# Kernel tuning notes

Measured on AMD Instinct MI355X. Metric: run time of the kernel, lower is better.

Reference implementation:

```python
import jax, jax.numpy as jnp
import numpy as np

H = 1024   # lstm_size
Z = 512    # z_size
E = 32     # subseq_embedding_dim
B = 256    # batch
T = 64     # length


def setup_inputs() -> dict:
    key = jax.random.key(0)
    ks = jax.random.split(key, 16)
    k = 1.0 / np.sqrt(H)  # PyTorch default uniform init bound
    u = lambda kk, shape: jax.random.uniform(kk, shape, jnp.float32, -k, k)
    return {
        "z": jax.random.normal(ks[0], (1, B, Z), jnp.float32),
        "targets": jax.random.normal(ks[1], (T, B, E), jnp.float32),
        "length": T,
        # LSTM layer 0 (input E -> H), gate order i,f,g,o as in PyTorch
        "W_ih0": u(ks[2], (4 * H, E)), "W_hh0": u(ks[3], (4 * H, H)),
        "b_ih0": u(ks[4], (4 * H,)),   "b_hh0": u(ks[5], (4 * H,)),
        # LSTM layer 1 (input H -> H)
        "W_ih1": u(ks[6], (4 * H, H)), "W_hh1": u(ks[7], (4 * H, H)),
        "b_ih1": u(ks[8], (4 * H,)),   "b_hh1": u(ks[9], (4 * H,)),
        # per-layer z -> initial hidden projections
        "Wz0": u(ks[10], (H, Z)), "bz0": u(ks[11], (H,)),
        "Wz1": u(ks[12], (H, Z)), "bz1": u(ks[13], (H,)),
        # output projection H -> E
        "Wp": u(ks[14], (E, H)), "bp": u(ks[15], (E,)),
    }


def _lstm_cell(x, h, c, W_ih, W_hh, b_ih, b_hh):
    # gates: [i, f, g, o] stacked along last dim (PyTorch layout)
    g = x @ W_ih.T + h @ W_hh.T + (b_ih + b_hh)
    i, f, gg, o = jnp.split(g, 4, axis=-1)
    c2 = jax.nn.sigmoid(f) * c + jax.nn.sigmoid(i) * jnp.tanh(gg)
    h2 = jax.nn.sigmoid(o) * jnp.tanh(c2)
    return h2, c2


def reference(z, targets, length, W_ih0, W_hh0, b_ih0, b_hh0,
              W_ih1, W_hh1, b_ih1, b_hh1, Wz0, bz0, Wz1, bz1, Wp, bp):
    batch = z.shape[1]
    emb = targets.shape[-1]
    z0 = z[0]  # (B, Z)
    # initial hidden = tanh(Linear(z)) per layer, initial cell = zeros
    h0 = jnp.tanh(z0 @ Wz0.T + bz0)
    h1 = jnp.tanh(z0 @ Wz1.T + bz1)
    c0 = jnp.zeros_like(h0)
    c1 = jnp.zeros_like(h1)

    # teacher-forced inputs: step 0 is zeros, step t uses targets[t-1] (detached)
    inputs = jnp.concatenate(
        [jnp.zeros((1, batch, emb), targets.dtype),
         jax.lax.stop_gradient(targets[: length - 1])], axis=0)

    def step(carry, x):
        h0, c0, h1, c1 = carry
        h0, c0 = _lstm_cell(x, h0, c0, W_ih0, W_hh0, b_ih0, b_hh0)
        h1, c1 = _lstm_cell(h0, h1, c1, W_ih1, W_hh1, b_ih1, b_hh1)
        out = h1 @ Wp.T + bp  # (B, E)
        return (h0, c0, h1, c1), out

    _, outs = jax.lax.scan(step, (h0, c0, h1, c1), inputs)
    return outs  # (length, B, E) == embedding_outputs
```

## Files before the change

### kernel.cpp

```cpp
#include <hip/hip_runtime.h>

#define TT 64
#define BB 256
#define HH 1024
#define ZZ 512
#define EE 32

#define NKB0 33
#define NKB1 64
#define NKBZ 16
#define NKBP 32

#define SLOTSH ((size_t)(HH / 16) * BB * 16)

typedef __attribute__((ext_vector_type(8))) short short8;
typedef __attribute__((ext_vector_type(4))) float f4;

__device__ __forceinline__ f4 mfma16(short8 a, short8 b, f4 c) {
  return __builtin_amdgcn_mfma_f32_16x16x32_bf16(a, b, c, 0, 0, 0);
}

__device__ __forceinline__ unsigned short f2bf(float f) {
  unsigned u = __builtin_bit_cast(unsigned, f);
  u = u + 0x7fffu + ((u >> 16) & 1u);
  return (unsigned short)(u >> 16);
}

__device__ __forceinline__ float sigm(float x) { return 1.0f / (1.0f + __expf(-x)); }
__device__ __forceinline__ float tanh_f(float x) { return 1.0f - 2.0f / (__expf(2.0f * x) + 1.0f); }

__device__ __forceinline__ short8 ld16(const short* p) { return *(const short8*)p; }

__device__ __forceinline__ short8 ld16_byp(const short* p) {
  union { unsigned long long u[2]; short8 v; } t;
  t.u[0] = __hip_atomic_load((const unsigned long long*)p, __ATOMIC_RELAXED, __HIP_MEMORY_SCOPE_AGENT);
  t.u[1] = __hip_atomic_load((const unsigned long long*)p + 1, __ATOMIC_RELAXED, __HIP_MEMORY_SCOPE_AGENT);
  return t.v;
}

__device__ __forceinline__ void st4_byp(short* p, unsigned v) {
  __hip_atomic_store((unsigned*)p, v, __ATOMIC_RELAXED, __HIP_MEMORY_SCOPE_AGENT);
}

__device__ __forceinline__ void btile_barrier(unsigned* bar, int btid, int jt, unsigned gen) {
  asm volatile("s_waitcnt vmcnt(0)" ::: "memory");
  __syncthreads();
  if (threadIdx.x == 0) {
    unsigned* base = bar + btid * (10 * 32);
    unsigned* leaf = base + (jt >> 3) * 32;
    unsigned* root = base + 8 * 32;
    unsigned* flag = base + 9 * 32;
    unsigned prev = __hip_atomic_fetch_add(leaf, 1u, __ATOMIC_RELAXED, __HIP_MEMORY_SCOPE_AGENT);
    if (prev == gen * 8u - 1u) {
      unsigned rp = __hip_atomic_fetch_add(root, 1u, __ATOMIC_RELAXED, __HIP_MEMORY_SCOPE_AGENT);
      if (rp == gen * 8u - 1u) {
        __hip_atomic_store(flag, gen, __ATOMIC_RELAXED, __HIP_MEMORY_SCOPE_AGENT);
      } else {
        while (__hip_atomic_load(flag, __ATOMIC_RELAXED, __HIP_MEMORY_SCOPE_AGENT) < gen)
          __builtin_amdgcn_s_sleep(1);
      }
    } else {
      while (__hip_atomic_load(flag, __ATOMIC_RELAXED, __HIP_MEMORY_SCOPE_AGENT) < gen)
        __builtin_amdgcn_s_sleep(1);
    }
  }
  __syncthreads();
}

__global__ void pack_all(
    const float* __restrict__ z, const float* __restrict__ tg,
    const float* __restrict__ Wih0, const float* __restrict__ Whh0,
    const float* __restrict__ Wih1, const float* __restrict__ Whh1,
    const float* __restrict__ Wz0, const float* __restrict__ Wz1,
    const float* __restrict__ Wp,
    short* __restrict__ W0P, short* __restrict__ W1P,
    short* __restrict__ WzP, short* __restrict__ WpP,
    short* __restrict__ zbf, short* __restrict__ Xbf)
{
  const int N0 = 64 * NKB0 * 4 * 64;
  const int N1 = 64 * NKB1 * 4 * 64;
  const int N2 = 32 * NKBZ * 4 * 64;
  const int N3 = NKBP * 2 * 64;
  const int N4 = (BB * ZZ) / 8;
  const int N5 = (TT * BB * EE) / 8;
  const int TOT = N0 + N1 + N2 + N3 + N4 + N5;
  for (int idx = blockIdx.x * blockDim.x + threadIdx.x; idx < TOT;
       idx += gridDim.x * blockDim.x) {
    int j = idx;
    short8 ov;
    if (j < N0) {
      const int l = j & 63, fc = (j >> 6) & 3, rest = j >> 8;
      const int kb = rest % NKB0, jt = rest / NKB0;
      const int row = fc * HH + jt * 16 + (l & 15);
      const int k0 = kb * 32 + ((l >> 4) * 8);
      #pragma unroll
      for (int i = 0; i < 8; ++i) {
        const int k = k0 + i;
        const float v = (k < HH) ? Whh0[(size_t)row * HH + k]
                                 : Wih0[(size_t)row * EE + (k - HH)];
        ov[i] = (short)f2bf(v);
      }
      *(short8*)(W0P + (size_t)j * 8) = ov;
      continue;
    }
    j -= N0;
    if (j < N1) {
      const int l = j & 63, fc = (j >> 6) & 3, rest = j >> 8;
      const int kb = rest & 63, jt = rest >> 6;
      const int row = fc * HH + jt * 16 + (l & 15);
      const int k0 = kb * 32 + ((l >> 4) * 8);
      #pragma unroll
      for (int i = 0; i < 8; ++i) {
        const int k = k0 + i;
        const float v = (k < HH) ? Wih1[(size_t)row * HH + k]
                                 : Whh1[(size_t)row * HH + (k - HH)];
        ov[i] = (short)f2bf(v);
      }
      *(short8*)(W1P + (size_t)j * 8) = ov;
      continue;
    }
    j -= N1;
    if (j < N2) {
      const int l = j & 63, fc = (j >> 6) & 3, rest = j >> 8;
      const int kb = rest & 15, ct = rest >> 4;
      const int col = ct * 64 + fc * 16 + (l & 15);
      const int lay = col >> 10, ch = col & (HH - 1);
      const int k0 = kb * 32 + ((l >> 4) * 8);
      const float* W = lay ? Wz1 : Wz0;
      #pragma unroll
      for (int i = 0; i < 8; ++i) ov[i] = (short)f2bf(W[(size_t)ch * ZZ + k0 + i]);
      *(short8*)(WzP + (size_t)j * 8) = ov;
      continue;
    }
    j -= N2;
    if (j < N3) {
      const int l = j & 63, fc = (j >> 6) & 1, kb = j >> 7;
      const int e = fc * 16 + (l & 15);
      const int k0 = kb * 32 + ((l >> 4) * 8);
      #pragma unroll
      for (int i = 0; i < 8; ++i) ov[i] = (short)f2bf(Wp[(size_t)e * HH + k0 + i]);
      *(short8*)(WpP + (size_t)j * 8) = ov;
      continue;
    }
    j -= N3;
    if (j < N4) {
      #pragma unroll
      for (int i = 0; i < 8; ++i) ov[i] = (short)f2bf(z[(size_t)j * 8 + i]);
      *(short8*)(zbf + (size_t)j * 8) = ov;
      continue;
    }
    j -= N4;
    {
      const int base = j * 8;
      const int t = base >> 13, rem = base & 8191;
      if (t == 0) {
        #pragma unroll
        for (int i = 0; i < 8; ++i) ov[i] = 0;
      } else {
        #pragma unroll
        for (int i = 0; i < 8; ++i) ov[i] = (short)f2bf(tg[(size_t)(t - 1) * 8192 + rem + i]);
      }
      *(short8*)(Xbf + (size_t)j * 8) = ov;
    }
  }
}

__global__ void __launch_bounds__(256, 1)
init_h(const short* __restrict__ WzP, const short* __restrict__ zbf,
       const float* __restrict__ bz0, const float* __restrict__ bz1,
       short* __restrict__ H0s0, short* __restrict__ H1s0)
{
  __shared__ float red[2][64][66];
  const int wg = blockIdx.x;
  const int btile = (wg >> 5) * 64;
  const int ct = wg & 31;
  const int tid = threadIdx.x;
  const int wv = tid >> 6, ln = tid & 63;
  const int lr = ln & 15, lk = (ln >> 4) * 8, hi4 = (ln >> 4) * 4;

  f4 acc[4][4];
  #pragma unroll
  for (int r = 0; r < 4; ++r)
    #pragma unroll
    for (int c = 0; c < 4; ++c) acc[r][c] = (f4)0.0f;

  #pragma unroll 2
  for (int i = 0; i < 4; ++i) {
    const int kb = wv + i * 4;
    short8 av[4], bv[4];
    const short* ap = zbf + (size_t)(btile + lr) * ZZ + kb * 32 + lk;
    #pragma unroll
    for (int r = 0; r < 4; ++r) av[r] = ld16(ap + (size_t)r * 16 * ZZ);
    const short* bp = WzP + ((size_t)(ct * NKBZ + kb) * 4) * 512 + ln * 8;
    #pragma unroll
    for (int c = 0; c < 4; ++c) bv[c] = ld16(bp + (size_t)c * 512);
    #pragma unroll
    for (int r = 0; r < 4; ++r)
      #pragma unroll
      for (int c = 0; c < 4; ++c) acc[r][c] = mfma16(av[r], bv[c], acc[r][c]);
  }

  if (wv < 2) {
    #pragma unroll
    for (int r = 0; r < 4; ++r)
      #pragma unroll
      for (int c = 0; c < 4; ++c)
        #pragma unroll
        for (int q = 0; q < 4; ++q)
          red[wv][r * 16 + hi4 + q][c * 16 + lr] = acc[r][c][q];
  }
  __syncthreads();
  if (wv >= 2) {
    #pragma unroll
    for (int r = 0; r < 4; ++r)
      #pragma unroll
      for (int c = 0; c < 4; ++c)
        #pragma unroll
        for (int q = 0; q < 4; ++q)
          red[wv - 2][r * 16 + hi4 + q][c * 16 + lr] += acc[r][c][q];
  }
  __syncthreads();

  const int c2 = tid & 63, rr = tid >> 6;
  #pragma unroll
  for (int k = 0; k < 16; ++k) {
    const int r = rr + k * 4;
    const int cg = ct * 64 + c2;
    const int lay = cg >> 10, ch = cg & (HH - 1);
    const float v = tanh_f(red[0][r][c2] + red[1][r][c2] + (lay ? bz1[ch] : bz0[ch]));
    short* dst = lay ? H1s0 : H0s0;
    dst[(size_t)(ch >> 4) * (BB * 16) + (size_t)(btile + r) * 16 + (ch & 15)] = (short)f2bf(v);
  }
}

template <bool BIG>
__global__ void __launch_bounds__(512, 1)
lstm_seq(const short* __restrict__ W0P, const short* __restrict__ W1P,
         const short* __restrict__ Xbf,
         short* __restrict__ H0, short* __restrict__ H1,
         short* __restrict__ H1a,
         const float* __restrict__ bi0, const float* __restrict__ bh0,
         const float* __restrict__ bi1, const float* __restrict__ bh1,
         unsigned* __restrict__ bar)
{
  __shared__ float red[4][64][66];
  const int wg = blockIdx.x;
  const int x = wg & 7;
  const int q = wg >> 3;
  const int jt = x + 8 * (q & 7);
  const int btid = q >> 3;
  const int btile = btid * 64;
  const int tid = threadIdx.x;
  const int wv = tid >> 6, ln = tid & 63;
  const int lr = ln & 15, lk = (ln >> 4) * 8, hi4 = (ln >> 4) * 4;

  const int u = tid & 15;
  const int rbase = tid >> 4;
  const int colg = jt * 16 + u;

  float bs0[4], bs1[4];
  #pragma unroll
  for (int g = 0; g < 4; ++g) {
    bs0[g] = bi0[g * HH + colg] + bh0[g * HH + colg];
    bs1[g] = bi1[g * HH + colg] + bh1[g * HH + colg];
  }

  const short* W0w = W0P + (size_t)jt * NKB0 * 4 * 512;
  const short* W1w = W1P + (size_t)jt * NKB1 * 4 * 512;

  const int aoff = (lk >> 4) * (BB * 16) + (btile + lr) * 16 + (lk & 15);
  const size_t ewi = (size_t)jt * (BB * 16) + u;

  float c0reg[2] = {0.0f, 0.0f}, c1reg[2] = {0.0f, 0.0f};

  for (int t = 0; t < TT; ++t) {
    const short* h0in = H0 + (size_t)(BIG ? t : (t & 1)) * SLOTSH;
    short* h0out      = H0 + (size_t)(BIG ? (t + 1) : ((t + 1) & 1)) * SLOTSH;
    const short* h1in = H1 + (size_t)(BIG ? t : (t & 1)) * SLOTSH;
    short* h1out      = H1 + (size_t)(BIG ? (t + 1) : ((t + 1) & 1)) * SLOTSH;

    f4 acc[4][4];
    #pragma unroll
    for (int r = 0; r < 4; ++r)
      #pragma unroll
      for (int c = 0; c < 4; ++c) acc[r][c] = (f4)0.0f;

    #pragma unroll
    for (int i = 0; i < 4; ++i) {
      const int kb = wv + 8 * i;
      short8 av[4], bv[4];
      const short* ap = h0in + (size_t)kb * 2 * (BB * 16) + aoff;
      #pragma unroll
      for (int r = 0; r < 4; ++r)
        av[r] = BIG ? ld16(ap + r * 256) : ld16_byp(ap + r * 256);
      const short* bp = W0w + (size_t)kb * 4 * 512 + ln * 8;
      #pragma unroll
      for (int c = 0; c < 4; ++c) bv[c] = ld16(bp + (size_t)c * 512);
      #pragma unroll
      for (int r = 0; r < 4; ++r)
        #pragma unroll
        for (int c = 0; c < 4; ++c) acc[r][c] = mfma16(av[r], bv[c], acc[r][c]);
    }
    if (wv == 0) {
      short8 av[4], bv[4];
      const short* ap = Xbf + (size_t)((size_t)t * BB + btile + lr) * EE + lk;
      #pragma unroll
      for (int r = 0; r < 4; ++r) av[r] = ld16(ap + (size_t)r * 16 * EE);
      const short* bp = W0w + (size_t)32 * 4 * 512 + ln * 8;
      #pragma unroll
      for (int c = 0; c < 4; ++c) bv[c] = ld16(bp + (size_t)c * 512);
      #pragma unroll
      for (int r = 0; r < 4; ++r)
        #pragma unroll
        for (int c = 0; c < 4; ++c) acc[r][c] = mfma16(av[r], bv[c], acc[r][c]);
    }

    if (wv < 4) {
      #pragma unroll
      for (int r = 0; r < 4; ++r)
        #pragma unroll
        for (int c = 0; c < 4; ++c)
          #pragma unroll
          for (int q2 = 0; q2 < 4; ++q2)
            red[wv][r * 16 + hi4 + q2][c * 16 + lr] = acc[r][c][q2];
    }
    __syncthreads();
    if (wv >= 4) {
      #pragma unroll
      for (int r = 0; r < 4; ++r)
        #pragma unroll
        for (int c = 0; c < 4; ++c)
          #pragma unroll
          for (int q2 = 0; q2 < 4; ++q2)
            red[wv - 4][r * 16 + hi4 + q2][c * 16 + lr] += acc[r][c][q2];
    }
    __syncthreads();

    #pragma unroll
    for (int k = 0; k < 2; ++k) {
      const int r = rbase + 32 * k;
      float s[4];
      #pragma unroll
      for (int g = 0; g < 4; ++g)
        s[g] = red[0][r][g * 16 + u] + red[1][r][g * 16 + u]
             + red[2][r][g * 16 + u] + red[3][r][g * 16 + u] + bs0[g];
      const float gi = sigm(s[0]), gf = sigm(s[1]);
      const float gg = tanh_f(s[2]), go = sigm(s[3]);
      c0reg[k] = gf * c0reg[k] + gi * gg;
      const unsigned hv = (unsigned)f2bf(go * tanh_f(c0reg[k]));
      const unsigned ov = (unsigned)__shfl_xor((int)hv, 1, 64);
      if ((tid & 1) == 0)
        st4_byp(h0out + ewi + (size_t)(btile + r) * 16, hv | (ov << 16));
    }

    btile_barrier(bar, btid, jt, (unsigned)(t + 1));

    #pragma unroll
    for (int r = 0; r < 4; ++r)
      #pragma unroll
      for (int c = 0; c < 4; ++c) acc[r][c] = (f4)0.0f;

    short8 a1[4][4];
    #pragma unroll
    for (int j = 0; j < 4; ++j) {
      const short* ap = h1in + (size_t)(wv + 8 * j) * 2 * (BB * 16) + aoff;
      #pragma unroll
      for (int r = 0; r < 4; ++r)
        a1[j][r] = BIG ? ld16(ap + r * 256) : ld16_byp(ap + r * 256);
    }

    #pragma unroll
    for (int i = 0; i < 4; ++i) {
      const int kb = wv + 8 * i;
      short8 av[4], bv[4];
      const short* ap = h0out + (size_t)kb * 2 * (BB * 16) + aoff;
      #pragma unroll
      for (int r = 0; r < 4; ++r)
        av[r] = BIG ? ld16(ap + r * 256) : ld16_byp(ap + r * 256);
      const short* bp = W1w + (size_t)kb * 4 * 512 + ln * 8;
      #pragma unroll
      for (int c = 0; c < 4; ++c) bv[c] = ld16(bp + (size_t)c * 512);
      #pragma unroll
      for (int r = 0; r < 4; ++r)
        #pragma unroll
        for (int c = 0; c < 4; ++c) acc[r][c] = mfma16(av[r], bv[c], acc[r][c]);
    }
    #pragma unroll
    for (int j = 0; j < 4; ++j) {
      const int kb = wv + 8 * j + 32;
      short8 bv[4];
      const short* bp = W1w + (size_t)kb * 4 * 512 + ln * 8;
      #pragma unroll
      for (int c = 0; c < 4; ++c) bv[c] = ld16(bp + (size_t)c * 512);
      #pragma unroll
      for (int r = 0; r < 4; ++r)
        #pragma unroll
        for (int c = 0; c < 4; ++c) acc[r][c] = mfma16(a1[j][r], bv[c], acc[r][c]);
    }

    if (wv < 4) {
      #pragma unroll
      for (int r = 0; r < 4; ++r)
        #pragma unroll
        for (int c = 0; c < 4; ++c)
          #pragma unroll
          for (int q2 = 0; q2 < 4; ++q2)
            red[wv][r * 16 + hi4 + q2][c * 16 + lr] = acc[r][c][q2];
    }
    __syncthreads();
    if (wv >= 4) {
      #pragma unroll
      for (int r = 0; r < 4; ++r)
        #pragma unroll
        for (int c = 0; c < 4; ++c)
          #pragma unroll
          for (int q2 = 0; q2 < 4; ++q2)
            red[wv - 4][r * 16 + hi4 + q2][c * 16 + lr] += acc[r][c][q2];
    }
    __syncthreads();

    #pragma unroll
    for (int k = 0; k < 2; ++k) {
      const int r = rbase + 32 * k;
      float s[4];
      #pragma unroll
      for (int g = 0; g < 4; ++g)
        s[g] = red[0][r][g * 16 + u] + red[1][r][g * 16 + u]
             + red[2][r][g * 16 + u] + red[3][r][g * 16 + u] + bs1[g];
      const float gi = sigm(s[0]), gf = sigm(s[1]);
      const float gg = tanh_f(s[2]), go = sigm(s[3]);
      c1reg[k] = gf * c1reg[k] + gi * gg;
      const unsigned hv = (unsigned)f2bf(go * tanh_f(c1reg[k]));
      const unsigned ov = (unsigned)__shfl_xor((int)hv, 1, 64);
      if ((tid & 1) == 0) {
        const size_t ci = ewi + (size_t)(btile + r) * 16;
        const unsigned pv = hv | (ov << 16);
        st4_byp(h1out + ci, pv);
        if (!BIG) st4_byp(H1a + (size_t)t * SLOTSH + ci, pv);
      }
    }
    __syncthreads();
  }
}

__global__ void __launch_bounds__(256, 1)
proj(const short* __restrict__ H1a, const short* __restrict__ WpP,
     const float* __restrict__ bp, float* __restrict__ out)
{
  __shared__ float red[2][64][34];
  const int rt = blockIdx.x * 64;
  const int tslot = rt >> 8;
  const int rb = rt & 255;
  const int tid = threadIdx.x;
  const int wv = tid >> 6, ln = tid & 63;
  const int lr = ln & 15, lk = (ln >> 4) * 8, hi4 = (ln >> 4) * 4;

  const short* base = H1a + (size_t)tslot * SLOTSH;
  const int aoff = (lk >> 4) * (BB * 16) + (rb + lr) * 16 + (lk & 15);

  f4 acc[4][2];
  #pragma unroll
  for (int r = 0; r < 4; ++r)
    #pragma unroll
    for (int c = 0; c < 2; ++c) acc[r][c] = (f4)0.0f;

  #pragma unroll 2
  for (int i = 0; i < 8; ++i) {
    const int kb = wv + i * 4;
    short8 av[4], bv[2];
    const short* ap = base + (size_t)kb * 2 * (BB * 16) + aoff;
    #pragma unroll
    for (int r = 0; r < 4; ++r) av[r] = ld16(ap + r * 256);
    const short* bq = WpP + (size_t)kb * 2 * 512 + ln * 8;
    #pragma unroll
    for (int c = 0; c < 2; ++c) bv[c] = ld16(bq + (size_t)c * 512);
    #pragma unroll
    for (int r = 0; r < 4; ++r)
      #pragma unroll
      for (int c = 0; c < 2; ++c) acc[r][c] = mfma16(av[r], bv[c], acc[r][c]);
  }

  if (wv < 2) {
    #pragma unroll
    for (int r = 0; r < 4; ++r)
      #pragma unroll
      for (int c = 0; c < 2; ++c)
        #pragma unroll
        for (int q = 0; q < 4; ++q)
          red[wv][r * 16 + hi4 + q][c * 16 + lr] = acc[r][c][q];
  }
  __syncthreads();
  if (wv >= 2) {
    #pragma unroll
    for (int r = 0; r < 4; ++r)
      #pragma unroll
      for (int c = 0; c < 2; ++c)
        #pragma unroll
        for (int q = 0; q < 4; ++q)
          red[wv - 2][r * 16 + hi4 + q][c * 16 + lr] += acc[r][c][q];
  }
  __syncthreads();

  const int ce = tid & 31, rr = tid >> 5;
  #pragma unroll
  for (int k = 0; k < 8; ++k) {
    const int r = rr + k * 8;
    out[(size_t)(rt + r) * EE + ce] = red[0][r][ce] + red[1][r][ce] + bp[ce];
  }
}

extern "C" void kernel_launch(void* const* d_in, const int* in_sizes, int n_in,
                              void* d_out, int out_size, void* d_ws, size_t ws_size,
                              hipStream_t stream) {
  const float* z    = (const float*)d_in[0];
  const float* tg   = (const float*)d_in[1];
  const float* Wih0 = (const float*)d_in[3];
  const float* Whh0 = (const float*)d_in[4];
  const float* bi0  = (const float*)d_in[5];
  const float* bh0  = (const float*)d_in[6];
  const float* Wih1 = (const float*)d_in[7];
  const float* Whh1 = (const float*)d_in[8];
  const float* bi1  = (const float*)d_in[9];
  const float* bh1  = (const float*)d_in[10];
  const float* Wz0  = (const float*)d_in[11];
  const float* bz0  = (const float*)d_in[12];
  const float* Wz1  = (const float*)d_in[13];
  const float* bz1  = (const float*)d_in[14];
  const float* Wp   = (const float*)d_in[15];
  const float* bpv  = (const float*)d_in[16];

  char* ws = (char*)d_ws;
  size_t off = 0;
  unsigned* bar = (unsigned*)(ws + off); off += 8192;
  short* W0P  = (short*)(ws + off); off += (size_t)64 * NKB0 * 4 * 512 * 2;
  short* W1P  = (short*)(ws + off); off += (size_t)64 * NKB1 * 4 * 512 * 2;
  short* WzP  = (short*)(ws + off); off += (size_t)32 * NKBZ * 4 * 512 * 2;
  short* WpP  = (short*)(ws + off); off += (size_t)NKBP * 2 * 512 * 2;
  short* zbf  = (short*)(ws + off); off += (size_t)BB * ZZ * 2;
  short* Xbf  = (short*)(ws + off); off += (size_t)TT * BB * EE * 2;

  const size_t seqB = (size_t)(TT + 1) * SLOTSH * 2;
  const size_t need_big = off + 2 * seqB;
  const size_t need_small = off + 2 * ((size_t)2 * SLOTSH * 2) + (size_t)TT * SLOTSH * 2;
  const bool big = (ws_size >= need_big);

  if (ws_size < need_small) return;

  hipMemsetAsync(bar, 0, 8192, stream);

  pack_all<<<dim3(1024), dim3(256), 0, stream>>>(z, tg, Wih0, Whh0, Wih1, Whh1,
                                                 Wz0, Wz1, Wp,
                                                 W0P, W1P, WzP, WpP, zbf, Xbf);
  if (big) {
    short* H0seq = (short*)(ws + off);
    short* H1seq = (short*)(ws + off + seqB);
    init_h<<<dim3(128), dim3(256), 0, stream>>>(WzP, zbf, bz0, bz1, H0seq, H1seq);
    lstm_seq<true><<<dim3(256), dim3(512), 0, stream>>>(W0P, W1P, Xbf, H0seq, H1seq,
                                                        (short*)nullptr,
                                                        bi0, bh0, bi1, bh1, bar);
    proj<<<dim3(256), dim3(256), 0, stream>>>(H1seq + SLOTSH, WpP, bpv, (float*)d_out);
  } else {
    short* H0pp = (short*)(ws + off);
    short* H1pp = H0pp + 2 * SLOTSH;
    short* H1a  = H1pp + 2 * SLOTSH;
    init_h<<<dim3(128), dim3(256), 0, stream>>>(WzP, zbf, bz0, bz1, H0pp, H1pp);
    lstm_seq<false><<<dim3(256), dim3(512), 0, stream>>>(W0P, W1P, Xbf, H0pp, H1pp,
                                                         H1a,
                                                         bi0, bh0, bi1, bh1, bar);
    proj<<<dim3(256), dim3(256), 0, stream>>>(H1a, WpP, bpv, (float*)d_out);
  }
}
```

Before: 910.9 us.

## Transpose LDS reduction buffer for vector stores, spread x-term MFMAs, prefetch W1 slice

```diff
diff --git a/kernel.cpp b/kernel.cpp
--- a/kernel.cpp
+++ b/kernel.cpp
@@ -243,7 +243,7 @@
          const float* __restrict__ bi1, const float* __restrict__ bh1,
          unsigned* __restrict__ bar)
 {
-  __shared__ float red[4][64][66];
+  __shared__ float red[4][64][68];
   const int wg = blockIdx.x;
   const int x = wg & 7;
   const int q = wg >> 3;
@@ -301,18 +301,19 @@
         #pragma unroll
         for (int c = 0; c < 4; ++c) acc[r][c] = mfma16(av[r], bv[c], acc[r][c]);
     }
-    if (wv == 0) {
-      short8 av[4], bv[4];
-      const short* ap = Xbf + (size_t)((size_t)t * BB + btile + lr) * EE + lk;
-      #pragma unroll
-      for (int r = 0; r < 4; ++r) av[r] = ld16(ap + (size_t)r * 16 * EE);
-      const short* bp = W0w + (size_t)32 * 4 * 512 + ln * 8;
-      #pragma unroll
-      for (int c = 0; c < 4; ++c) bv[c] = ld16(bp + (size_t)c * 512);
-      #pragma unroll
-      for (int r = 0; r < 4; ++r)
-        #pragma unroll
-        for (int c = 0; c < 4; ++c) acc[r][c] = mfma16(av[r], bv[c], acc[r][c]);
+
+    {
+      const short* xbase = Xbf + (size_t)((size_t)t * BB + btile + lr) * EE + lk;
+      const short* bp32 = W0w + (size_t)32 * 4 * 512 + ln * 8;
+      #pragma unroll
+      for (int r = 0; r < 4; ++r)
+        #pragma unroll
+        for (int c = 0; c < 4; ++c)
+          if (((r * 4 + c) >> 1) == wv) {
+            const short8 av = ld16(xbase + (size_t)r * 16 * EE);
+            const short8 bv = ld16(bp32 + (size_t)c * 512);
+            acc[r][c] = mfma16(av, bv, acc[r][c]);
+          }
     }
 
     if (wv < 4) {
@@ -320,19 +321,19 @@
       for (int r = 0; r < 4; ++r)
         #pragma unroll
         for (int c = 0; c < 4; ++c)
-          #pragma unroll
-          for (int q2 = 0; q2 < 4; ++q2)
-            red[wv][r * 16 + hi4 + q2][c * 16 + lr] = acc[r][c][q2];
+          *(f4*)&red[wv][c * 16 + lr][r * 16 + hi4] = acc[r][c];
     }
     __syncthreads();
     if (wv >= 4) {
       #pragma unroll
       for (int r = 0; r < 4; ++r)
         #pragma unroll
-        for (int c = 0; c < 4; ++c)
-          #pragma unroll
-          for (int q2 = 0; q2 < 4; ++q2)
-            red[wv - 4][r * 16 + hi4 + q2][c * 16 + lr] += acc[r][c][q2];
+        for (int c = 0; c < 4; ++c) {
+          f4* p = (f4*)&red[wv - 4][c * 16 + lr][r * 16 + hi4];
+          f4 v = *p;
+          v += acc[r][c];
+          *p = v;
+        }
     }
     __syncthreads();
 
@@ -342,8 +343,8 @@
       float s[4];
       #pragma unroll
       for (int g = 0; g < 4; ++g)
-        s[g] = red[0][r][g * 16 + u] + red[1][r][g * 16 + u]
-             + red[2][r][g * 16 + u] + red[3][r][g * 16 + u] + bs0[g];
+        s[g] = red[0][g * 16 + u][r] + red[1][g * 16 + u][r]
+             + red[2][g * 16 + u][r] + red[3][g * 16 + u][r] + bs0[g];
       const float gi = sigm(s[0]), gf = sigm(s[1]);
       const float gg = tanh_f(s[2]), go = sigm(s[3]);
       c0reg[k] = gf * c0reg[k] + gi * gg;
@@ -353,6 +354,13 @@
         st4_byp(h0out + ewi + (size_t)(btile + r) * 16, hv | (ov << 16));
     }
 
+    short8 bv0[4];
+    {
+      const short* bp0 = W1w + (size_t)wv * 4 * 512 + ln * 8;
+      #pragma unroll
+      for (int c = 0; c < 4; ++c) bv0[c] = ld16(bp0 + (size_t)c * 512);
+    }
+
     btile_barrier(bar, btid, jt, (unsigned)(t + 1));
 
     #pragma unroll
@@ -377,9 +385,14 @@
       #pragma unroll
       for (int r = 0; r < 4; ++r)
         av[r] = BIG ? ld16(ap + r * 256) : ld16_byp(ap + r * 256);
-      const short* bp = W1w + (size_t)kb * 4 * 512 + ln * 8;
-      #pragma unroll
-      for (int c = 0; c < 4; ++c) bv[c] = ld16(bp + (size_t)c * 512);
+      if (i == 0) {
+        #pragma unroll
+        for (int c = 0; c < 4; ++c) bv[c] = bv0[c];
+      } else {
+        const short* bp = W1w + (size_t)kb * 4 * 512 + ln * 8;
+        #pragma unroll
+        for (int c = 0; c < 4; ++c) bv[c] = ld16(bp + (size_t)c * 512);
+      }
       #pragma unroll
       for (int r = 0; r < 4; ++r)
         #pragma unroll
@@ -403,19 +416,19 @@
       for (int r = 0; r < 4; ++r)
         #pragma unroll
         for (int c = 0; c < 4; ++c)
-          #pragma unroll
-          for (int q2 = 0; q2 < 4; ++q2)
-            red[wv][r * 16 + hi4 + q2][c * 16 + lr] = acc[r][c][q2];
+          *(f4*)&red[wv][c * 16 + lr][r * 16 + hi4] = acc[r][c];
     }
     __syncthreads();
     if (wv >= 4) {
       #pragma unroll
       for (int r = 0; r < 4; ++r)
         #pragma unroll
-        for (int c = 0; c < 4; ++c)
-          #pragma unroll
-          for (int q2 = 0; q2 < 4; ++q2)
-            red[wv - 4][r * 16 + hi4 + q2][c * 16 + lr] += acc[r][c][q2];
+        for (int c = 0; c < 4; ++c) {
+          f4* p = (f4*)&red[wv - 4][c * 16 + lr][r * 16 + hi4];
+          f4 v = *p;
+          v += acc[r][c];
+          *p = v;
+        }
     }
     __syncthreads();
 
@@ -425,8 +438,8 @@
       float s[4];
       #pragma unroll
       for (int g = 0; g < 4; ++g)
-        s[g] = red[0][r][g * 16 + u] + red[1][r][g * 16 + u]
-             + red[2][r][g * 16 + u] + red[3][r][g * 16 + u] + bs1[g];
+        s[g] = red[0][g * 16 + u][r] + red[1][g * 16 + u][r]
+             + red[2][g * 16 + u][r] + red[3][g * 16 + u][r] + bs1[g];
       const float gi = sigm(s[0]), gf = sigm(s[1]);
       const float gg = tanh_f(s[2]), go = sigm(s[3]);
       c1reg[k] = gf * c1reg[k] + gi * gg;
```

Result: no change. 898.6 us (-1.4%).
